# Performance work log

Hardware: AMD Instinct MI355X
Metric: run time of the kernel (lower is better)

## Reference

```python
import jax, jax.numpy as jnp
import numpy as np

H, R, B = 8192, 4, 64


def glorot(key, shape):
    return jax.random.uniform(key, shape, minval=-1.0, maxval=1.0) * jnp.sqrt(2.0 / sum(shape))


def setup_inputs() -> dict:
    key = jax.random.key(0)
    k1, k2, k3, k4, kh, kx = jax.random.split(key, 6)
    return {
        "h": jax.random.normal(kh, (B, H), dtype=jnp.float32),
        "x": jax.random.normal(kx, (B, H), dtype=jnp.float32),
        "a_diag": glorot(k1, (H,)).astype(jnp.float32),
        "p_vec": glorot(k2, (H, R)).astype(jnp.float32),
        "q_vec": glorot(k3, (H, R)).astype(jnp.float32),
        "b_mat": glorot(k4, (H, H)).astype(jnp.float32),
    }


def reference(h, x, a_diag, p_vec, q_vec, b_mat):
    # Faithful to the source: explicitly materialize the dense DPLR matrix
    # a_dplr = diag(a_diag) + p q^T  (H x H), then a_dplr @ h + b_mat.T @ x.
    a_dplr = jnp.diag(a_diag) + p_vec @ q_vec.T  # (H, H)
    # Batched over leading dim: (a_dplr @ h_i) == h @ a_dplr.T ; (b_mat.T @ x_i) == x @ b_mat
    return h @ a_dplr.T + x @ b_mat  # (B, H)
```

## Files before the change

kernel.cpp:

```cpp
#include <hip/hip_runtime.h>
#include <hip/hip_bf16.h>


#define HDIM 8192
#define BDIM 64
#define RDIM 4
#define KSPLIT 16
#define KSLAB 512
#define JGRP 256
#define NKSTEP (KSLAB / 32)

typedef short short8 __attribute__((ext_vector_type(8)));
typedef float f32x4 __attribute__((ext_vector_type(4)));

__device__ __forceinline__ unsigned f2bf(float f) {
  unsigned u = __float_as_uint(f);
  unsigned r = u + 0x7fffu + ((u >> 16) & 1u);
  return r >> 16;
}

__device__ __forceinline__ float bf2f(unsigned short u) {
  return __uint_as_float(((unsigned)u) << 16);
}

__global__ void prep_x_kernel(const float* __restrict__ x,
                              unsigned short* __restrict__ xb) {
  size_t i = ((size_t)blockIdx.x * blockDim.x + threadIdx.x) * 8;
  f32x4 v0 = *(const f32x4*)(x + i);
  f32x4 v1 = *(const f32x4*)(x + i + 4);
  union { unsigned short u[8]; short8 s; } o;
#pragma unroll
  for (int e = 0; e < 4; ++e) {
    o.u[e] = (unsigned short)f2bf(v0[e]);
    o.u[4 + e] = (unsigned short)f2bf(v1[e]);
  }
  *(short8*)(xb + i) = o.s;
}

__global__ void hq_kernel(const float* __restrict__ h,
                          const float* __restrict__ q,
                          float* __restrict__ hq) {
  const int b = blockIdx.x, t = threadIdx.x;
  const float* hrow = h + (size_t)b * HDIM;
  f32x4 s = {0.f, 0.f, 0.f, 0.f};
  for (int k = t; k < HDIM; k += 256) {
    float hv = hrow[k];
    f32x4 qv = *(const f32x4*)(q + (size_t)k * RDIM);
    s += hv * qv;
  }
  __shared__ f32x4 red[256];
  red[t] = s;
  __syncthreads();
  for (int off = 128; off > 0; off >>= 1) {
    if (t < off) red[t] += red[t + off];
    __syncthreads();
  }
  if (t == 0) *(f32x4*)(hq + (size_t)b * RDIM) = red[0];
}

__global__ __launch_bounds__(512, 4)
void dplr_main(const float* __restrict__ bmat,
               const unsigned short* __restrict__ xb,
               unsigned short* __restrict__ part) {
  __shared__ __align__(16) unsigned short xs[BDIM * KSLAB];

  const int t    = threadIdx.x;
  const int lane = t & 63;
  const int w    = t >> 6;
  const int c    = lane & 15;
  const int kgrp = lane >> 4;

  const int jg = blockIdx.x & 31;
  const int ks = blockIdx.x >> 5;
  const int k0 = ks * KSLAB;

  {
    const int row = t >> 3;
    const int kq0 = (t & 7) * 8;
    const unsigned short* src = xb + (size_t)row * HDIM + k0 + kq0 * 8;
#pragma unroll
    for (int i = 0; i < 8; ++i) {
      const int g  = row * (KSLAB / 8) + kq0 + i;
      const int gs = g ^ (row & 7);
      *(short8*)&xs[gs * 8] = *(const short8*)(src + i * 8);
    }
  }
  __syncthreads();

  const int j0 = jg * JGRP + w * 32;
  const float* b0 = bmat + (size_t)(k0 + kgrp * 8) * HDIM + j0 + c;

  f32x4 acc[4][2];
#pragma unroll
  for (int mt = 0; mt < 4; ++mt)
#pragma unroll
    for (int ct = 0; ct < 2; ++ct) acc[mt][ct] = (f32x4){0.f, 0.f, 0.f, 0.f};

  float fA0[8], fA1[8], fB0[8], fB1[8];

  auto issue = [&](int ki, float* g0, float* g1) {
#pragma unroll
    for (int i = 0; i < 8; ++i) {
      const float* p = b0 + (size_t)(ki * 32 + i) * HDIM;
      g0[i] = p[0];
      g1[i] = p[16];
    }
  };
  auto conv_mfma = [&](int ki, const float* g0, const float* g1) {
    union { unsigned short u[8]; short8 s; } bf0, bf1;
#pragma unroll
    for (int i = 0; i < 8; ++i) {
      bf0.u[i] = (unsigned short)f2bf(g0[i]);
      bf1.u[i] = (unsigned short)f2bf(g1[i]);
    }
#pragma unroll
    for (int mt = 0; mt < 4; ++mt) {
      const int row = mt * 16 + c;
      const int g   = row * (KSLAB / 8) + ki * 4 + kgrp;
      const int gs  = g ^ (row & 7);
      short8 af = *(const short8*)&xs[gs * 8];
      acc[mt][0] = __builtin_amdgcn_mfma_f32_16x16x32_bf16(af, bf0.s, acc[mt][0], 0, 0, 0);
      acc[mt][1] = __builtin_amdgcn_mfma_f32_16x16x32_bf16(af, bf1.s, acc[mt][1], 0, 0, 0);
    }
  };

  issue(0, fA0, fA1);
  for (int ki = 0; ki < NKSTEP; ki += 2) {
    issue(ki + 1, fB0, fB1);
    conv_mfma(ki, fA0, fA1);
    if (ki + 2 < NKSTEP) issue(ki + 2, fA0, fA1);
    conv_mfma(ki + 1, fB0, fB1);
  }

  unsigned short* pb = part + (size_t)ks * BDIM * HDIM;
#pragma unroll
  for (int mt = 0; mt < 4; ++mt)
#pragma unroll
    for (int ct = 0; ct < 2; ++ct)
#pragma unroll
      for (int r = 0; r < 4; ++r) {
        const int row = mt * 16 + kgrp * 4 + r;
        const int col = j0 + ct * 16 + c;
        pb[(size_t)row * HDIM + col] = (unsigned short)f2bf(acc[mt][ct][r]);
      }
}

__global__ __launch_bounds__(256)
void combine_kernel(const unsigned short* __restrict__ part,
                    const float* __restrict__ h,
                    const float* __restrict__ adiag,
                    const float* __restrict__ pvec,
                    const float* __restrict__ hq,
                    float* __restrict__ out) {
  const int tid  = blockIdx.x * 256 + threadIdx.x;
  const int base = tid * 8;
  const int row  = base >> 13;
  const int j    = base & 8191;

  float s[8];
#pragma unroll
  for (int e = 0; e < 8; ++e) s[e] = 0.f;
  const unsigned short* pp = part + (size_t)row * HDIM + j;
#pragma unroll
  for (int ks = 0; ks < KSPLIT; ++ks) {
    union { unsigned short u[8]; short8 v; } pv;
    pv.v = *(const short8*)(pp + (size_t)ks * BDIM * HDIM);
#pragma unroll
    for (int e = 0; e < 8; ++e) s[e] += bf2f(pv.u[e]);
  }
  const f32x4 hv0 = *(const f32x4*)(h + (size_t)row * HDIM + j);
  const f32x4 hv1 = *(const f32x4*)(h + (size_t)row * HDIM + j + 4);
  const f32x4 a0  = *(const f32x4*)(adiag + j);
  const f32x4 a1  = *(const f32x4*)(adiag + j + 4);
  const f32x4 hqv = *(const f32x4*)(hq + (size_t)row * RDIM);

  float res[8];
#pragma unroll
  for (int e = 0; e < 4; ++e) {
    const f32x4 pv = *(const f32x4*)(pvec + (size_t)(j + e) * RDIM);
    res[e] = s[e] + hv0[e] * a0[e] +
             hqv[0] * pv[0] + hqv[1] * pv[1] + hqv[2] * pv[2] + hqv[3] * pv[3];
  }
#pragma unroll
  for (int e = 0; e < 4; ++e) {
    const f32x4 pv = *(const f32x4*)(pvec + (size_t)(j + 4 + e) * RDIM);
    res[4 + e] = s[4 + e] + hv1[e] * a1[e] +
                 hqv[0] * pv[0] + hqv[1] * pv[1] + hqv[2] * pv[2] + hqv[3] * pv[3];
  }
  f32x4 o0 = {res[0], res[1], res[2], res[3]};
  f32x4 o1 = {res[4], res[5], res[6], res[7]};
  *(f32x4*)(out + (size_t)row * HDIM + j) = o0;
  *(f32x4*)(out + (size_t)row * HDIM + j + 4) = o1;
}

extern "C" void kernel_launch(void* const* d_in, const int* in_sizes, int n_in,
                              void* d_out, int out_size, void* d_ws, size_t ws_size,
                              hipStream_t stream) {
  const float* h     = (const float*)d_in[0];
  const float* x     = (const float*)d_in[1];
  const float* adiag = (const float*)d_in[2];
  const float* pvec  = (const float*)d_in[3];
  const float* qvec  = (const float*)d_in[4];
  const float* bmat  = (const float*)d_in[5];
  float* out = (float*)d_out;

  unsigned short* xb = (unsigned short*)d_ws;
  float* hqbuf = (float*)((char*)d_ws + ((size_t)1 << 20));
  unsigned short* part = (unsigned short*)((char*)d_ws + ((size_t)2 << 20));

  prep_x_kernel<<<(BDIM * HDIM / 8) / 256, 256, 0, stream>>>(x, xb);
  hq_kernel<<<BDIM, 256, 0, stream>>>(h, qvec, hqbuf);
  dplr_main<<<KSPLIT * 32, 512, 0, stream>>>(bmat, xb, part);
  combine_kernel<<<(BDIM * HDIM / 8) / 256, 256, 0, stream>>>(part, h, adiag, pvec, hqbuf, out);
}
```

Before: 77.80 us.

## Switch main GEMM to 32x32x16 MFMA and merge x-prep with hq kernel

The main split-K kernel now uses 32x32x16 bf16 MFMA tiles, so each wave covers 64 rows by 32 columns with two accumulators instead of eight 16x16 tiles. Each B element is loaded once per lane, with 16 rows per k-step instead of 8 rows at two column offsets. This cuts the number of MFMA issues and LDS fragment reads. Separately, the x-to-bf16 conversion is folded into the hq reduction kernel, removing one launch. The larger MFMA has longer latency and a different output layout, and the merged prep kernel runs only 64 blocks for the conversion.

```diff
diff --git a/kernel.cpp b/kernel.cpp
--- a/kernel.cpp
+++ b/kernel.cpp
@@ -12,6 +12,7 @@
 
 typedef short short8 __attribute__((ext_vector_type(8)));
 typedef float f32x4 __attribute__((ext_vector_type(4)));
+typedef float f32x16 __attribute__((ext_vector_type(16)));
 
 __device__ __forceinline__ unsigned f2bf(float f) {
   unsigned u = __float_as_uint(f);
@@ -23,24 +24,30 @@
   return __uint_as_float(((unsigned)u) << 16);
 }
 
-__global__ void prep_x_kernel(const float* __restrict__ x,
-                              unsigned short* __restrict__ xb) {
-  size_t i = ((size_t)blockIdx.x * blockDim.x + threadIdx.x) * 8;
-  f32x4 v0 = *(const f32x4*)(x + i);
-  f32x4 v1 = *(const f32x4*)(x + i + 4);
-  union { unsigned short u[8]; short8 s; } o;
-#pragma unroll
-  for (int e = 0; e < 4; ++e) {
-    o.u[e] = (unsigned short)f2bf(v0[e]);
-    o.u[4 + e] = (unsigned short)f2bf(v1[e]);
-  }
-  *(short8*)(xb + i) = o.s;
-}
-
-__global__ void hq_kernel(const float* __restrict__ h,
-                          const float* __restrict__ q,
-                          float* __restrict__ hq) {
+__global__ __launch_bounds__(256)
+void prep_hq_kernel(const float* __restrict__ x,
+                    const float* __restrict__ h,
+                    const float* __restrict__ q,
+                    unsigned short* __restrict__ xb,
+                    float* __restrict__ hq) {
   const int b = blockIdx.x, t = threadIdx.x;
+  {
+    const float* xrow = x + (size_t)b * HDIM;
+    unsigned short* xo = xb + (size_t)b * HDIM;
+#pragma unroll
+    for (int i = 0; i < 4; ++i) {
+      const int base = (t * 4 + i) * 8;
+      f32x4 v0 = *(const f32x4*)(xrow + base);
+      f32x4 v1 = *(const f32x4*)(xrow + base + 4);
+      union { unsigned short u[8]; short8 s; } o;
+#pragma unroll
+      for (int e = 0; e < 4; ++e) {
+        o.u[e] = (unsigned short)f2bf(v0[e]);
+        o.u[4 + e] = (unsigned short)f2bf(v1[e]);
+      }
+      *(short8*)(xo + base) = o.s;
+    }
+  }
   const float* hrow = h + (size_t)b * HDIM;
   f32x4 s = {0.f, 0.f, 0.f, 0.f};
   for (int k = t; k < HDIM; k += 256) {
@@ -67,8 +74,8 @@
   const int t    = threadIdx.x;
   const int lane = t & 63;
   const int w    = t >> 6;
-  const int c    = lane & 15;
-  const int kgrp = lane >> 4;
+  const int c32  = lane & 31;
+  const int kh   = lane >> 5;
 
   const int jg = blockIdx.x & 31;
   const int ks = blockIdx.x >> 5;
@@ -88,61 +95,57 @@
   __syncthreads();
 
   const int j0 = jg * JGRP + w * 32;
-  const float* b0 = bmat + (size_t)(k0 + kgrp * 8) * HDIM + j0 + c;
-
-  f32x4 acc[4][2];
-#pragma unroll
-  for (int mt = 0; mt < 4; ++mt)
-#pragma unroll
-    for (int ct = 0; ct < 2; ++ct) acc[mt][ct] = (f32x4){0.f, 0.f, 0.f, 0.f};
-
-  float fA0[8], fA1[8], fB0[8], fB1[8];
-
-  auto issue = [&](int ki, float* g0, float* g1) {
-#pragma unroll
-    for (int i = 0; i < 8; ++i) {
-      const float* p = b0 + (size_t)(ki * 32 + i) * HDIM;
-      g0[i] = p[0];
-      g1[i] = p[16];
-    }
+  const float* b0 = bmat + (size_t)(k0 + kh * 8) * HDIM + j0 + c32;
+
+  f32x16 acc[2];
+#pragma unroll
+  for (int mt = 0; mt < 2; ++mt)
+#pragma unroll
+    for (int r = 0; r < 16; ++r) acc[mt][r] = 0.f;
+
+  float fA[16], fB[16];
+
+  auto issue = [&](int ki, float* g) {
+#pragma unroll
+    for (int s = 0; s < 2; ++s)
+#pragma unroll
+      for (int i = 0; i < 8; ++i)
+        g[s * 8 + i] = b0[(size_t)(ki * 32 + s * 16 + i) * HDIM];
   };
-  auto conv_mfma = [&](int ki, const float* g0, const float* g1) {
-    union { unsigned short u[8]; short8 s; } bf0, bf1;
-#pragma unroll
-    for (int i = 0; i < 8; ++i) {
-      bf0.u[i] = (unsigned short)f2bf(g0[i]);
-      bf1.u[i] = (unsigned short)f2bf(g1[i]);
-    }
-#pragma unroll
-    for (int mt = 0; mt < 4; ++mt) {
-      const int row = mt * 16 + c;
-      const int g   = row * (KSLAB / 8) + ki * 4 + kgrp;
-      const int gs  = g ^ (row & 7);
-      short8 af = *(const short8*)&xs[gs * 8];
-      acc[mt][0] = __builtin_amdgcn_mfma_f32_16x16x32_bf16(af, bf0.s, acc[mt][0], 0, 0, 0);
-      acc[mt][1] = __builtin_amdgcn_mfma_f32_16x16x32_bf16(af, bf1.s, acc[mt][1], 0, 0, 0);
+  auto conv_mfma = [&](int ki, const float* g) {
+#pragma unroll
+    for (int s = 0; s < 2; ++s) {
+      union { unsigned short u[8]; short8 v; } bf;
+#pragma unroll
+      for (int i = 0; i < 8; ++i) bf.u[i] = (unsigned short)f2bf(g[s * 8 + i]);
+#pragma unroll
+      for (int mt = 0; mt < 2; ++mt) {
+        const int row = mt * 32 + c32;
+        const int gg  = row * (KSLAB / 8) + ki * 4 + s * 2 + kh;
+        const int gs  = gg ^ (row & 7);
+        short8 af = *(const short8*)&xs[gs * 8];
+        acc[mt] = __builtin_amdgcn_mfma_f32_32x32x16_bf16(af, bf.v, acc[mt], 0, 0, 0);
+      }
     }
   };
 
-  issue(0, fA0, fA1);
+  issue(0, fA);
   for (int ki = 0; ki < NKSTEP; ki += 2) {
-    issue(ki + 1, fB0, fB1);
-    conv_mfma(ki, fA0, fA1);
-    if (ki + 2 < NKSTEP) issue(ki + 2, fA0, fA1);
-    conv_mfma(ki + 1, fB0, fB1);
+    issue(ki + 1, fB);
+    conv_mfma(ki, fA);
+    if (ki + 2 < NKSTEP) issue(ki + 2, fA);
+    conv_mfma(ki + 1, fB);
   }
 
   unsigned short* pb = part + (size_t)ks * BDIM * HDIM;
 #pragma unroll
-  for (int mt = 0; mt < 4; ++mt)
-#pragma unroll
-    for (int ct = 0; ct < 2; ++ct)
-#pragma unroll
-      for (int r = 0; r < 4; ++r) {
-        const int row = mt * 16 + kgrp * 4 + r;
-        const int col = j0 + ct * 16 + c;
-        pb[(size_t)row * HDIM + col] = (unsigned short)f2bf(acc[mt][ct][r]);
-      }
+  for (int mt = 0; mt < 2; ++mt)
+#pragma unroll
+    for (int reg = 0; reg < 16; ++reg) {
+      const int row = mt * 32 + (reg & 3) + 8 * (reg >> 2) + 4 * kh;
+      const int col = j0 + c32;
+      pb[(size_t)row * HDIM + col] = (unsigned short)f2bf(acc[mt][reg]);
+    }
 }
 
 __global__ __launch_bounds__(256)
@@ -208,8 +211,7 @@
   float* hqbuf = (float*)((char*)d_ws + ((size_t)1 << 20));
   unsigned short* part = (unsigned short*)((char*)d_ws + ((size_t)2 << 20));
 
-  prep_x_kernel<<<(BDIM * HDIM / 8) / 256, 256, 0, stream>>>(x, xb);
-  hq_kernel<<<BDIM, 256, 0, stream>>>(h, qvec, hqbuf);
+  prep_hq_kernel<<<BDIM, 256, 0, stream>>>(x, h, qvec, xb, hqbuf);
   dplr_main<<<KSPLIT * 32, 512, 0, stream>>>(bmat, xb, part);
   combine_kernel<<<(BDIM * HDIM / 8) / 256, 256, 0, stream>>>(part, h, adiag, pvec, hqbuf, out);
 }
```

After: 76.29 us. No clear change (-1.9%).
